# Kernel tuning notes

Hardware: AMD Instinct MI355X
Metric: run time of the kernel (lower is better)

Reference implementation:

```python
import jax, jax.numpy as jnp
import numpy as np

ALPHA = 0.2  # LeakyReLU negative slope


def setup_inputs() -> dict:
    key = jax.random.key(0)
    k1, k2, k3, k4 = jax.random.split(key, 4)
    B, N, Fin, Fout = 8, 2048, 256, 256
    h = jax.random.normal(k1, (B, N, Fin), dtype=jnp.float32)
    # random 0/1 adjacency with guaranteed self-loops so every row has a neighbor
    adj = jax.random.randint(k2, (N, N), 0, 2).astype(jnp.float32)
    adj = jnp.maximum(adj, jnp.eye(N, dtype=jnp.float32))
    # xavier_uniform with gain=1.414
    def xavier(k, shape, gain=1.414):
        fan_in, fan_out = shape[0], shape[1]
        a = gain * np.sqrt(6.0 / (fan_in + fan_out))
        return jax.random.uniform(k, shape, dtype=jnp.float32, minval=-a, maxval=a)
    W = xavier(k3, (Fin, Fout))
    a = xavier(k4, (2 * Fout, 1))
    return {"h": h, "adj_matrix": adj, "W": W, "a": a}


def reference(h, adj_matrix, W, a):
    # h: [B, N, Fin], adj_matrix: [N, N], W: [Fin, Fout], a: [2*Fout, 1]
    Fout = W.shape[1]
    Wh = jnp.einsum("bnf,fo->bno", h, W)            # [B, N, Fout]
    a1, a2 = a[:Fout, 0], a[Fout:, 0]                 # split additive attention vector
    # e[b,i,j] = leakyrelu(Wh[b,i]@a1 + Wh[b,j]@a2) — equals concat([Wh_i,Wh_j])@a
    s1 = Wh @ a1                                      # [B, N]
    s2 = Wh @ a2                                      # [B, N]
    e = s1[:, :, None] + s2[:, None, :]               # [B, N, N]
    e = jnp.where(e >= 0, e, ALPHA * e)               # LeakyReLU
    e = jnp.where(adj_matrix[None] == 0, -jnp.inf, e)  # mask non-edges
    attention = jax.nn.softmax(e, axis=-1)            # [B, N, N]
    # dropout is identity in eval mode (training=False)
    h_prime = jnp.einsum("bij,bjo->bio", attention, Wh)
    return h_prime
```

## Files before the change

### kernel.cpp

```cpp
#include <hip/hip_runtime.h>
#include <cstdint>

#define NN 2048
#define LOG2E 1.4426950408889634f

typedef __attribute__((ext_vector_type(8))) short bf16x8;
typedef __attribute__((ext_vector_type(4))) float f32x4;

__device__ __forceinline__ unsigned short f2bf(float x){
  union { float f; unsigned u; } v; v.f = x;
  unsigned r = v.u + 0x7FFFu + ((v.u >> 16) & 1u);
  return (unsigned short)(r >> 16);
}
__device__ __forceinline__ unsigned pack2(float a, float b){
  return (unsigned)f2bf(a) | ((unsigned)f2bf(b) << 16);
}
__device__ __forceinline__ unsigned permpack(unsigned hi, unsigned lo){
  return __builtin_amdgcn_perm(hi, lo, 0x07060302u);
}

__global__ __launch_bounds__(256) void k_prep(const float* __restrict__ adj,
                                              const float* __restrict__ W,
                                              unsigned long long* __restrict__ ab,
                                              unsigned short* __restrict__ Wt){
  int tid = threadIdx.x;
  if (blockIdx.x < 2048){
    int i = blockIdx.x;
    int w = tid >> 6, lane = tid & 63;
    #pragma unroll
    for (int seg = 0; seg < 8; seg++){
      int j = seg * 256 + tid;
      unsigned long long m = __ballot(adj[(size_t)i * NN + j] != 0.0f);
      if (lane == 0) ab[i * 32 + seg * 4 + w] = m;
    }
  } else {
    int g = (blockIdx.x - 2048) * 256 + tid;
    int o = g >> 8, k = g & 255;
    Wt[g] = f2bf(W[k * 256 + o]);
  }
}

__global__ __launch_bounds__(512, 2) void k_fused_gemm(const float* __restrict__ h,
                                                       const unsigned short* __restrict__ Wt,
                                                       const float* __restrict__ a,
                                                       unsigned short* __restrict__ WhT,
                                                       float* __restrict__ s1c,
                                                       float* __restrict__ s2c){
  __shared__ __align__(16) unsigned char As[2 * 8192];
  __shared__ __align__(16) unsigned short Ts[256 * 72];
  __shared__ float s1p[8][64], s2p[8][64];
  const int tid = threadIdx.x;
  const int r0 = blockIdx.x * 64;
  const int b  = r0 >> 11;
  const int i0 = r0 & (NN - 1);
  const int w = tid >> 6, lane = tid & 63, lhi = lane >> 4, llo = lane & 15;
  const int wc = w * 32;
  const int sit = w >> 1, skk = w & 1;
  const int srow = sit * 16 + llo;
  const int skol = skk * 32 + lhi * 8;

  f32x4 acc[4][2];
  #pragma unroll
  for (int i = 0; i < 4; i++)
    #pragma unroll
    for (int j = 0; j < 2; j++){ acc[i][j][0]=0.f; acc[i][j][1]=0.f; acc[i][j][2]=0.f; acc[i][j][3]=0.f; }

  float4 hv[4][2];
  #pragma unroll
  for (int t = 0; t < 4; t++){
    const float* hp = h + (size_t)(r0 + srow) * 256 + t * 64 + skol;
    hv[t][0] = *(const float4*)hp;
    hv[t][1] = *(const float4*)(hp + 4);
  }

  auto loadB = [&](int k0, bf16x8* dst){
    #pragma unroll
    for (int ot = 0; ot < 2; ot++)
      #pragma unroll
      for (int kk = 0; kk < 2; kk++)
        dst[ot * 2 + kk] = *(const bf16x8*)(Wt + (size_t)(wc + ot * 16 + llo) * 256 + k0 + kk * 32 + lhi * 8);
  };
  bf16x8 bfr[2][4];
  loadB(0, bfr[0]);

  #pragma unroll
  for (int t = 0; t < 4; t++){
    uint4 q = make_uint4(pack2(hv[t][0].x, hv[t][0].y), pack2(hv[t][0].z, hv[t][0].w),
                         pack2(hv[t][1].x, hv[t][1].y), pack2(hv[t][1].z, hv[t][1].w));
    *(uint4*)&As[(t & 1) * 8192 + w * 1024 + lane * 16] = q;
    __syncthreads();
    if (t < 3) loadB((t + 1) * 64, bfr[(t + 1) & 1]);
    bf16x8 af[2][4];
    #pragma unroll
    for (int kk = 0; kk < 2; kk++)
      #pragma unroll
      for (int it = 0; it < 4; it++)
        af[kk][it] = *(const bf16x8*)&As[(t & 1) * 8192 + (it * 2 + kk) * 1024 + lane * 16];
    #pragma unroll
    for (int kk = 0; kk < 2; kk++)
      #pragma unroll
      for (int it = 0; it < 4; it++)
        #pragma unroll
        for (int ot = 0; ot < 2; ot++)
          acc[it][ot] = __builtin_amdgcn_mfma_f32_16x16x32_bf16(af[kk][it], bfr[t & 1][ot * 2 + kk], acc[it][ot], 0, 0, 0);
  }

  float a1v[2], a2v[2];
  #pragma unroll
  for (int ot = 0; ot < 2; ot++){
    a1v[ot] = a[wc + ot * 16 + llo] * LOG2E;
    a2v[ot] = a[256 + wc + ot * 16 + llo] * LOG2E;
  }
  #pragma unroll
  for (int it = 0; it < 4; it++){
    #pragma unroll
    for (int q = 0; q < 4; q++){
      float p1 = acc[it][0][q] * a1v[0] + acc[it][1][q] * a1v[1];
      float p2 = acc[it][0][q] * a2v[0] + acc[it][1][q] * a2v[1];
      #pragma unroll
      for (int o = 1; o < 16; o <<= 1){ p1 += __shfl_xor(p1, o); p2 += __shfl_xor(p2, o); }
      if (llo == 0){
        s1p[w][it * 16 + lhi * 4 + q] = p1;
        s2p[w][it * 16 + lhi * 4 + q] = p2;
      }
    }
  }

  #pragma unroll
  for (int it = 0; it < 4; it++){
    #pragma unroll
    for (int ot = 0; ot < 2; ot++){
      int o = wc + ot * 16 + llo;
      uint2 u = make_uint2(pack2(acc[it][ot][0], acc[it][ot][1]),
                           pack2(acc[it][ot][2], acc[it][ot][3]));
      *(uint2*)&Ts[o * 72 + it * 16 + lhi * 4] = u;
    }
  }
  __syncthreads();

  if (tid < 64){
    float t1 = 0.f, t2 = 0.f;
    #pragma unroll
    for (int g = 0; g < 8; g++){ t1 += s1p[g][tid]; t2 += s2p[g][tid]; }
    s1c[r0 + tid] = t1;
    s2c[r0 + tid] = t2;
  }
  #pragma unroll
  for (int p = 0; p < 4; p++){
    int o = p * 64 + (tid >> 3), col = (tid & 7) * 8;
    *(uint4*)(WhT + (size_t)(b * 256 + o) * 2048 + i0 + col) = *(const uint4*)&Ts[o * 72 + col];
  }
}

__global__ __launch_bounds__(512, 2) void k_attn(const float* __restrict__ s1c,
                                                 const float* __restrict__ s2c,
                                                 const unsigned short* __restrict__ WhT,
                                                 const unsigned long long* __restrict__ ab,
                                                 float* __restrict__ out){
  __shared__ __align__(16) float s2s[2048];
  __shared__ __align__(16) unsigned char PsB[2 * 8192];
  __shared__ __align__(16) unsigned char bitsB[64 * 264];
  __shared__ float s1s[64], lin[64], red[8], rsp[8][64];
  const int tid = threadIdx.x;
  const int bid = blockIdx.x;
  const int b = bid & 7, i0 = (bid >> 3) * 64;
  const int w = tid >> 6, lane = tid & 63, lhi = lane >> 4, llo = lane & 15;
  const int wc = w * 32;
  const int sit = w >> 1, skk = w & 1;
  const int prow = sit * 16 + llo;

  float4 v = ((const float4*)(s2c + (size_t)b * NN))[tid];
  ((float4*)s2s)[tid] = v;
  float vmax = fmaxf(fmaxf(v.x, v.y), fmaxf(v.z, v.w));
  #pragma unroll
  for (int o = 32; o; o >>= 1) vmax = fmaxf(vmax, __shfl_xor(vmax, o));
  if (lane == 0) red[w] = vmax;
  if (tid < 64) s1s[tid] = s1c[(size_t)b * NN + i0 + tid];
  #pragma unroll
  for (int k = 0; k < 4; k++){
    int g = k * 512 + tid;
    unsigned long long mw = ab[(size_t)i0 * 32 + g];
    *(unsigned long long*)&bitsB[(g >> 5) * 264 + (g & 31) * 8] = mw;
  }
  __syncthreads();
  float m2 = red[0];
  #pragma unroll
  for (int g = 1; g < 8; g++) m2 = fmaxf(m2, red[g]);

  const float s1v = s1s[prow];
  const float xm = s1v + m2;
  const float mv = fmaxf(xm, 0.2f * xm);
  const float c1 = s1v - mv;
  const float c2 = 0.2f * s1v - mv;
  float rs = 0.f;

  f32x4 acc[4][2];
  #pragma unroll
  for (int i = 0; i < 4; i++)
    #pragma unroll
    for (int j = 0; j < 2; j++){ acc[i][j][0]=0.f; acc[i][j][1]=0.f; acc[i][j][2]=0.f; acc[i][j][3]=0.f; }

  auto loadB = [&](int j0, bf16x8* dst){
    #pragma unroll
    for (int ot = 0; ot < 2; ot++)
      #pragma unroll
      for (int kk = 0; kk < 2; kk++)
        dst[ot * 2 + kk] = *(const bf16x8*)(WhT + (size_t)(b * 256 + wc + ot * 16 + llo) * 2048 + j0 + kk * 32 + lhi * 8);
  };

  unsigned puq[4];
  auto computeP = [&](int tn){
    unsigned bits = bitsB[prow * 264 + tn * 8 + skk * 4 + lhi];
    const float* sp = &s2s[tn * 64 + skk * 32 + lhi * 8];
    float4 xa = *(const float4*)sp;
    float4 xb = *(const float4*)(sp + 4);
    float xs[8] = {xa.x, xa.y, xa.z, xa.w, xb.x, xb.y, xb.z, xb.w};
    unsigned pu[8];
    #pragma unroll
    for (int e = 0; e < 8; e++){
      float s2v = xs[e];
      float y = fmaxf(s2v + c1, __builtin_fmaf(0.2f, s2v, c2));
      float p = __builtin_amdgcn_exp2f(y);
      unsigned m = ((bits >> e) & 1u) ? 0xFFFF0000u : 0u;
      unsigned u = __float_as_uint(p) & m;
      rs += __uint_as_float(u);
      pu[e] = u;
    }
    puq[0] = permpack(pu[1], pu[0]); puq[1] = permpack(pu[3], pu[2]);
    puq[2] = permpack(pu[5], pu[4]); puq[3] = permpack(pu[7], pu[6]);
  };

  auto stageBody = [&](int t, int BUF, bf16x8* curB, bf16x8* nxtB, bool last){
    *(uint4*)&PsB[BUF * 8192 + w * 1024 + lane * 16] = *(uint4*)&puq[0];
    __syncthreads();
    if (!last) loadB((t + 1) * 64, nxtB);
    bf16x8 af[2][4];
    #pragma unroll
    for (int kk = 0; kk < 2; kk++)
      #pragma unroll
      for (int it = 0; it < 4; it++)
        af[kk][it] = *(const bf16x8*)&PsB[BUF * 8192 + (it * 2 + kk) * 1024 + lane * 16];
    if (!last) computeP(t + 1);
    #pragma unroll
    for (int kk = 0; kk < 2; kk++)
      #pragma unroll
      for (int it = 0; it < 4; it++)
        #pragma unroll
        for (int ot = 0; ot < 2; ot++)
          acc[it][ot] = __builtin_amdgcn_mfma_f32_16x16x32_bf16(af[kk][it], curB[ot * 2 + kk], acc[it][ot], 0, 0, 0);
  };

  bf16x8 bA[4], bB[4];
  loadB(0, bA);
  computeP(0);
  for (int t2 = 0; t2 < 32; t2 += 2){
    stageBody(t2,     0, bA, bB, false);
    stageBody(t2 + 1, 1, bB, bA, t2 + 1 == 31);
  }

  rs += __shfl_xor(rs, 16);
  rs += __shfl_xor(rs, 32);
  if (lhi == 0) rsp[w][prow] = rs;
  __syncthreads();
  if (tid < 64){
    int it = tid >> 4;
    lin[tid] = 1.0f / (rsp[it * 2][tid] + rsp[it * 2 + 1][tid]);
  }
  __syncthreads();

  #pragma unroll
  for (int it = 0; it < 4; it++){
    #pragma unroll
    for (int ot = 0; ot < 2; ot++){
      int col = wc + ot * 16 + llo;
      #pragma unroll
      for (int q = 0; q < 4; q++){
        int row = it * 16 + lhi * 4 + q;
        out[(size_t)(b * NN + i0 + row) * 256 + col] = acc[it][ot][q] * lin[row];
      }
    }
  }
}

extern "C" void kernel_launch(void* const* d_in, const int* in_sizes, int n_in,
                              void* d_out, int out_size, void* d_ws, size_t ws_size,
                              hipStream_t stream) {
  const float* h   = (const float*)d_in[0];
  const float* adj = (const float*)d_in[1];
  const float* W   = (const float*)d_in[2];
  const float* a   = (const float*)d_in[3];
  float* out = (float*)d_out;

  char* ws = (char*)d_ws;
  unsigned short* WhT      = (unsigned short*)(ws);
  unsigned short* Wt       = (unsigned short*)(ws + 8388608);
  unsigned long long* ab   = (unsigned long long*)(ws + 8519680);
  float* s1c               = (float*)(ws + 9043968);
  float* s2c               = (float*)(ws + 9109504);

  hipLaunchKernelGGL(k_prep,       dim3(2304), dim3(256), 0, stream, adj, W, ab, Wt);
  hipLaunchKernelGGL(k_fused_gemm, dim3(256),  dim3(512), 0, stream, h, Wt, a, WhT, s1c, s2c);
  hipLaunchKernelGGL(k_attn,       dim3(256),  dim3(512), 0, stream, s1c, s2c, WhT, ab, out);
}
```

Measured before the change: 135.2 us.

## Halve row tile to 32 rows per block, doubling grid size

Both the projection GEMM and the attention kernel now process 32 query rows per block instead of 64, so 512 blocks are launched instead of 256. Each wave computes half the rows and the staging layout splits each fragment across two waves. Launch bounds rise to 4 blocks per CU. The aim is to fill the MI355X's 256 CUs with more than one block each and improve latency hiding. The cost is that each WhT tile is reloaded by twice as many blocks, and each block does less MFMA work per barrier.

```diff
diff --git a/kernel.cpp b/kernel.cpp
--- a/kernel.cpp
+++ b/kernel.cpp
@@ -40,38 +40,36 @@
   }
 }
 
-__global__ __launch_bounds__(512, 2) void k_fused_gemm(const float* __restrict__ h,
+__global__ __launch_bounds__(512, 4) void k_fused_gemm(const float* __restrict__ h,
                                                        const unsigned short* __restrict__ Wt,
                                                        const float* __restrict__ a,
                                                        unsigned short* __restrict__ WhT,
                                                        float* __restrict__ s1c,
                                                        float* __restrict__ s2c){
-  __shared__ __align__(16) unsigned char As[2 * 8192];
-  __shared__ __align__(16) unsigned short Ts[256 * 72];
-  __shared__ float s1p[8][64], s2p[8][64];
+  __shared__ __align__(16) unsigned char As[2 * 4096];
+  __shared__ __align__(16) unsigned short Ts[256 * 40];
+  __shared__ float s1p[8][32], s2p[8][32];
   const int tid = threadIdx.x;
-  const int r0 = blockIdx.x * 64;
+  const int r0 = blockIdx.x * 32;
   const int b  = r0 >> 11;
   const int i0 = r0 & (NN - 1);
   const int w = tid >> 6, lane = tid & 63, lhi = lane >> 4, llo = lane & 15;
   const int wc = w * 32;
-  const int sit = w >> 1, skk = w & 1;
+  const int sit = w >> 2, skk = (w >> 1) & 1, sh2 = w & 1;
+  const int sfrag = sit * 2 + skk;
   const int srow = sit * 16 + llo;
-  const int skol = skk * 32 + lhi * 8;
-
-  f32x4 acc[4][2];
-  #pragma unroll
-  for (int i = 0; i < 4; i++)
+  const int skol = skk * 32 + lhi * 8 + sh2 * 4;
+
+  f32x4 acc[2][2];
+  #pragma unroll
+  for (int i = 0; i < 2; i++)
     #pragma unroll
     for (int j = 0; j < 2; j++){ acc[i][j][0]=0.f; acc[i][j][1]=0.f; acc[i][j][2]=0.f; acc[i][j][3]=0.f; }
 
-  float4 hv[4][2];
-  #pragma unroll
-  for (int t = 0; t < 4; t++){
-    const float* hp = h + (size_t)(r0 + srow) * 256 + t * 64 + skol;
-    hv[t][0] = *(const float4*)hp;
-    hv[t][1] = *(const float4*)(hp + 4);
-  }
+  float4 hv[4];
+  #pragma unroll
+  for (int t = 0; t < 4; t++)
+    hv[t] = *(const float4*)(h + (size_t)(r0 + srow) * 256 + t * 64 + skol);
 
   auto loadB = [&](int k0, bf16x8* dst){
     #pragma unroll
@@ -85,21 +83,20 @@
 
   #pragma unroll
   for (int t = 0; t < 4; t++){
-    uint4 q = make_uint4(pack2(hv[t][0].x, hv[t][0].y), pack2(hv[t][0].z, hv[t][0].w),
-                         pack2(hv[t][1].x, hv[t][1].y), pack2(hv[t][1].z, hv[t][1].w));
-    *(uint4*)&As[(t & 1) * 8192 + w * 1024 + lane * 16] = q;
+    *(uint2*)&As[(t & 1) * 4096 + sfrag * 1024 + lane * 16 + sh2 * 8] =
+        make_uint2(pack2(hv[t].x, hv[t].y), pack2(hv[t].z, hv[t].w));
     __syncthreads();
     if (t < 3) loadB((t + 1) * 64, bfr[(t + 1) & 1]);
-    bf16x8 af[2][4];
+    bf16x8 af[2][2];
     #pragma unroll
     for (int kk = 0; kk < 2; kk++)
       #pragma unroll
-      for (int it = 0; it < 4; it++)
-        af[kk][it] = *(const bf16x8*)&As[(t & 1) * 8192 + (it * 2 + kk) * 1024 + lane * 16];
+      for (int it = 0; it < 2; it++)
+        af[kk][it] = *(const bf16x8*)&As[(t & 1) * 4096 + (it * 2 + kk) * 1024 + lane * 16];
     #pragma unroll
     for (int kk = 0; kk < 2; kk++)
       #pragma unroll
-      for (int it = 0; it < 4; it++)
+      for (int it = 0; it < 2; it++)
         #pragma unroll
         for (int ot = 0; ot < 2; ot++)
           acc[it][ot] = __builtin_amdgcn_mfma_f32_16x16x32_bf16(af[kk][it], bfr[t & 1][ot * 2 + kk], acc[it][ot], 0, 0, 0);
@@ -112,7 +109,7 @@
     a2v[ot] = a[256 + wc + ot * 16 + llo] * LOG2E;
   }
   #pragma unroll
-  for (int it = 0; it < 4; it++){
+  for (int it = 0; it < 2; it++){
     #pragma unroll
     for (int q = 0; q < 4; q++){
       float p1 = acc[it][0][q] * a1v[0] + acc[it][1][q] * a1v[1];
@@ -127,18 +124,18 @@
   }
 
   #pragma unroll
-  for (int it = 0; it < 4; it++){
+  for (int it = 0; it < 2; it++){
     #pragma unroll
     for (int ot = 0; ot < 2; ot++){
       int o = wc + ot * 16 + llo;
-      uint2 u = make_uint2(pack2(acc[it][ot][0], acc[it][ot][1]),
-                           pack2(acc[it][ot][2], acc[it][ot][3]));
-      *(uint2*)&Ts[o * 72 + it * 16 + lhi * 4] = u;
+      *(uint2*)&Ts[o * 40 + it * 16 + lhi * 4] =
+          make_uint2(pack2(acc[it][ot][0], acc[it][ot][1]),
+                     pack2(acc[it][ot][2], acc[it][ot][3]));
     }
   }
   __syncthreads();
 
-  if (tid < 64){
+  if (tid < 32){
     float t1 = 0.f, t2 = 0.f;
     #pragma unroll
     for (int g = 0; g < 8; g++){ t1 += s1p[g][tid]; t2 += s2p[g][tid]; }
@@ -146,27 +143,29 @@
     s2c[r0 + tid] = t2;
   }
   #pragma unroll
-  for (int p = 0; p < 4; p++){
-    int o = p * 64 + (tid >> 3), col = (tid & 7) * 8;
-    *(uint4*)(WhT + (size_t)(b * 256 + o) * 2048 + i0 + col) = *(const uint4*)&Ts[o * 72 + col];
-  }
-}
-
-__global__ __launch_bounds__(512, 2) void k_attn(const float* __restrict__ s1c,
+  for (int p = 0; p < 2; p++){
+    int idx = p * 512 + tid;
+    int o = idx >> 2, col = (idx & 3) * 8;
+    *(uint4*)(WhT + (size_t)(b * 256 + o) * 2048 + i0 + col) = *(const uint4*)&Ts[o * 40 + col];
+  }
+}
+
+__global__ __launch_bounds__(512, 4) void k_attn(const float* __restrict__ s1c,
                                                  const float* __restrict__ s2c,
                                                  const unsigned short* __restrict__ WhT,
                                                  const unsigned long long* __restrict__ ab,
                                                  float* __restrict__ out){
   __shared__ __align__(16) float s2s[2048];
-  __shared__ __align__(16) unsigned char PsB[2 * 8192];
-  __shared__ __align__(16) unsigned char bitsB[64 * 264];
-  __shared__ float s1s[64], lin[64], red[8], rsp[8][64];
+  __shared__ __align__(16) unsigned char PsB[2 * 4096];
+  __shared__ __align__(16) unsigned char bitsB[32 * 264];
+  __shared__ float s1s[32], lin[32], red[8], rsp[8][32];
   const int tid = threadIdx.x;
   const int bid = blockIdx.x;
-  const int b = bid & 7, i0 = (bid >> 3) * 64;
+  const int b = bid & 7, i0 = (bid >> 3) * 32;
   const int w = tid >> 6, lane = tid & 63, lhi = lane >> 4, llo = lane & 15;
   const int wc = w * 32;
-  const int sit = w >> 1, skk = w & 1;
+  const int sit = w >> 2, skk = (w >> 1) & 1, sh2 = w & 1;
+  const int sfrag = sit * 2 + skk;
   const int prow = sit * 16 + llo;
 
   float4 v = ((const float4*)(s2c + (size_t)b * NN))[tid];
@@ -175,9 +174,9 @@
   #pragma unroll
   for (int o = 32; o; o >>= 1) vmax = fmaxf(vmax, __shfl_xor(vmax, o));
   if (lane == 0) red[w] = vmax;
-  if (tid < 64) s1s[tid] = s1c[(size_t)b * NN + i0 + tid];
-  #pragma unroll
-  for (int k = 0; k < 4; k++){
+  if (tid < 32) s1s[tid] = s1c[(size_t)b * NN + i0 + tid];
+  #pragma unroll
+  for (int k = 0; k < 2; k++){
     int g = k * 512 + tid;
     unsigned long long mw = ab[(size_t)i0 * 32 + g];
     *(unsigned long long*)&bitsB[(g >> 5) * 264 + (g & 31) * 8] = mw;
@@ -194,9 +193,9 @@
   const float c2 = 0.2f * s1v - mv;
   float rs = 0.f;
 
-  f32x4 acc[4][2];
-  #pragma unroll
-  for (int i = 0; i < 4; i++)
+  f32x4 acc[2][2];
+  #pragma unroll
+  for (int i = 0; i < 2; i++)
     #pragma unroll
     for (int j = 0; j < 2; j++){ acc[i][j][0]=0.f; acc[i][j][1]=0.f; acc[i][j][2]=0.f; acc[i][j][3]=0.f; }
 
@@ -208,16 +207,15 @@
         dst[ot * 2 + kk] = *(const bf16x8*)(WhT + (size_t)(b * 256 + wc + ot * 16 + llo) * 2048 + j0 + kk * 32 + lhi * 8);
   };
 
-  unsigned puq[4];
+  unsigned puq[2];
   auto computeP = [&](int tn){
-    unsigned bits = bitsB[prow * 264 + tn * 8 + skk * 4 + lhi];
-    const float* sp = &s2s[tn * 64 + skk * 32 + lhi * 8];
+    unsigned bits = (bitsB[prow * 264 + tn * 8 + skk * 4 + lhi] >> (sh2 * 4)) & 0xFu;
+    const float* sp = &s2s[tn * 64 + skk * 32 + lhi * 8 + sh2 * 4];
     float4 xa = *(const float4*)sp;
-    float4 xb = *(const float4*)(sp + 4);
-    float xs[8] = {xa.x, xa.y, xa.z, xa.w, xb.x, xb.y, xb.z, xb.w};
-    unsigned pu[8];
-    #pragma unroll
-    for (int e = 0; e < 8; e++){
+    float xs[4] = {xa.x, xa.y, xa.z, xa.w};
+    unsigned pu[4];
+    #pragma unroll
+    for (int e = 0; e < 4; e++){
       float s2v = xs[e];
       float y = fmaxf(s2v + c1, __builtin_fmaf(0.2f, s2v, c2));
       float p = __builtin_amdgcn_exp2f(y);
@@ -227,24 +225,23 @@
       pu[e] = u;
     }
     puq[0] = permpack(pu[1], pu[0]); puq[1] = permpack(pu[3], pu[2]);
-    puq[2] = permpack(pu[5], pu[4]); puq[3] = permpack(pu[7], pu[6]);
   };
 
   auto stageBody = [&](int t, int BUF, bf16x8* curB, bf16x8* nxtB, bool last){
-    *(uint4*)&PsB[BUF * 8192 + w * 1024 + lane * 16] = *(uint4*)&puq[0];
+    *(uint2*)&PsB[BUF * 4096 + sfrag * 1024 + lane * 16 + sh2 * 8] = make_uint2(puq[0], puq[1]);
     __syncthreads();
     if (!last) loadB((t + 1) * 64, nxtB);
-    bf16x8 af[2][4];
+    bf16x8 af[2][2];
     #pragma unroll
     for (int kk = 0; kk < 2; kk++)
       #pragma unroll
-      for (int it = 0; it < 4; it++)
-        af[kk][it] = *(const bf16x8*)&PsB[BUF * 8192 + (it * 2 + kk) * 1024 + lane * 16];
+      for (int it = 0; it < 2; it++)
+        af[kk][it] = *(const bf16x8*)&PsB[BUF * 4096 + (it * 2 + kk) * 1024 + lane * 16];
     if (!last) computeP(t + 1);
     #pragma unroll
     for (int kk = 0; kk < 2; kk++)
       #pragma unroll
-      for (int it = 0; it < 4; it++)
+      for (int it = 0; it < 2; it++)
         #pragma unroll
         for (int ot = 0; ot < 2; ot++)
           acc[it][ot] = __builtin_amdgcn_mfma_f32_16x16x32_bf16(af[kk][it], curB[ot * 2 + kk], acc[it][ot], 0, 0, 0);
@@ -262,14 +259,14 @@
   rs += __shfl_xor(rs, 32);
   if (lhi == 0) rsp[w][prow] = rs;
   __syncthreads();
-  if (tid < 64){
-    int it = tid >> 4;
-    lin[tid] = 1.0f / (rsp[it * 2][tid] + rsp[it * 2 + 1][tid]);
+  if (tid < 32){
+    int g0 = (tid >> 4) * 4;
+    lin[tid] = 1.0f / (rsp[g0][tid] + rsp[g0 + 1][tid] + rsp[g0 + 2][tid] + rsp[g0 + 3][tid]);
   }
   __syncthreads();
 
   #pragma unroll
-  for (int it = 0; it < 4; it++){
+  for (int it = 0; it < 2; it++){
     #pragma unroll
     for (int ot = 0; ot < 2; ot++){
       int col = wc + ot * 16 + llo;
@@ -299,6 +296,6 @@
   float* s2c               = (float*)(ws + 9109504);
 
   hipLaunchKernelGGL(k_prep,       dim3(2304), dim3(256), 0, stream, adj, W, ab, Wt);
-  hipLaunchKernelGGL(k_fused_gemm, dim3(256),  dim3(512), 0, stream, h, Wt, a, WhT, s1c, s2c);
-  hipLaunchKernelGGL(k_attn,       dim3(256),  dim3(512), 0, stream, s1c, s2c, WhT, ab, out);
-}
+  hipLaunchKernelGGL(k_fused_gemm, dim3(512),  dim3(512), 0, stream, h, Wt, a, WhT, s1c, s2c);
+  hipLaunchKernelGGL(k_attn,       dim3(512),  dim3(512), 0, stream, s1c, s2c, WhT, ab, out);
+}
```

Result: slower. 157.3 us (+16.3%).

## Vectorize adjacency bitpacking and double attention k-tile per barrier

Applied to the files above, without the earlier changes.

The prep kernel now reads the adjacency with float4 loads and builds the bitmask through shuffle-based nibble merging, with each block handling four rows. That cuts the block count from 2048 to 512 mask blocks. The attention kernel processes 128 columns per stage instead of 64, with two P sub-tiles per LDS buffer. This halves the number of __syncthreads and gives the WhT loads more time to land. The cost is doubled B-fragment registers and LDS for P, which may lower occupancy or cause spills under the 512x2 launch bound.

```diff
diff --git a/kernel.cpp b/kernel.cpp
--- a/kernel.cpp
+++ b/kernel.cpp
@@ -23,18 +23,29 @@
                                               const float* __restrict__ W,
                                               unsigned long long* __restrict__ ab,
                                               unsigned short* __restrict__ Wt){
-  int tid = threadIdx.x;
-  if (blockIdx.x < 2048){
-    int i = blockIdx.x;
-    int w = tid >> 6, lane = tid & 63;
-    #pragma unroll
-    for (int seg = 0; seg < 8; seg++){
-      int j = seg * 256 + tid;
-      unsigned long long m = __ballot(adj[(size_t)i * NN + j] != 0.0f);
-      if (lane == 0) ab[i * 32 + seg * 4 + w] = m;
+  const int tid = threadIdx.x;
+  const int bid = blockIdx.x;
+  if (bid < 512){
+    const int lane = tid & 63;
+    unsigned* ab32 = (unsigned*)ab;
+    #pragma unroll
+    for (int r = 0; r < 4; r++){
+      const int row = bid * 4 + r;
+      #pragma unroll
+      for (int part = 0; part < 2; part++){
+        float4 v = ((const float4*)(adj + (size_t)row * NN))[part * 256 + tid];
+        unsigned n = (v.x != 0.f ? 1u : 0u) | (v.y != 0.f ? 2u : 0u)
+                   | (v.z != 0.f ? 4u : 0u) | (v.w != 0.f ? 8u : 0u);
+        unsigned m;
+        m = __shfl_xor(n, 1); n = (lane & 1) ? (m | (n << 4))  : (n | (m << 4));
+        m = __shfl_xor(n, 2); n = (lane & 2) ? (m | (n << 8))  : (n | (m << 8));
+        m = __shfl_xor(n, 4); n = (lane & 4) ? (m | (n << 16)) : (n | (m << 16));
+        if ((lane & 7) == 0)
+          ab32[row * 64 + part * 32 + (tid >> 3)] = n;
+      }
     }
   } else {
-    int g = (blockIdx.x - 2048) * 256 + tid;
+    int g = (bid - 512) * 256 + tid;
     int o = g >> 8, k = g & 255;
     Wt[g] = f2bf(W[k * 256 + o]);
   }
@@ -158,7 +169,7 @@
                                                  const unsigned long long* __restrict__ ab,
                                                  float* __restrict__ out){
   __shared__ __align__(16) float s2s[2048];
-  __shared__ __align__(16) unsigned char PsB[2 * 8192];
+  __shared__ __align__(16) unsigned char PsB[2 * 16384];
   __shared__ __align__(16) unsigned char bitsB[64 * 264];
   __shared__ float s1s[64], lin[64], red[8], rsp[8][64];
   const int tid = threadIdx.x;
@@ -167,6 +178,7 @@
   const int w = tid >> 6, lane = tid & 63, lhi = lane >> 4, llo = lane & 15;
   const int wc = w * 32;
   const int sit = w >> 1, skk = w & 1;
+  const int sfrag = sit * 2 + skk;
   const int prow = sit * 16 + llo;
 
   float4 v = ((const float4*)(s2c + (size_t)b * NN))[tid];
@@ -202,14 +214,16 @@
 
   auto loadB = [&](int j0, bf16x8* dst){
     #pragma unroll
-    for (int ot = 0; ot < 2; ot++)
-      #pragma unroll
-      for (int kk = 0; kk < 2; kk++)
-        dst[ot * 2 + kk] = *(const bf16x8*)(WhT + (size_t)(b * 256 + wc + ot * 16 + llo) * 2048 + j0 + kk * 32 + lhi * 8);
+    for (int jh = 0; jh < 2; jh++)
+      #pragma unroll
+      for (int ot = 0; ot < 2; ot++)
+        #pragma unroll
+        for (int kk = 0; kk < 2; kk++)
+          dst[jh * 4 + ot * 2 + kk] = *(const bf16x8*)(WhT + (size_t)(b * 256 + wc + ot * 16 + llo) * 2048 + j0 + jh * 64 + kk * 32 + lhi * 8);
   };
 
-  unsigned puq[4];
-  auto computeP = [&](int tn){
+  unsigned puq[8];
+  auto computeP = [&](int tn, unsigned* pq){
     unsigned bits = bitsB[prow * 264 + tn * 8 + skk * 4 + lhi];
     const float* sp = &s2s[tn * 64 + skk * 32 + lhi * 8];
     float4 xa = *(const float4*)sp;
@@ -226,21 +240,22 @@
       rs += __uint_as_float(u);
       pu[e] = u;
     }
-    puq[0] = permpack(pu[1], pu[0]); puq[1] = permpack(pu[3], pu[2]);
-    puq[2] = permpack(pu[5], pu[4]); puq[3] = permpack(pu[7], pu[6]);
+    pq[0] = permpack(pu[1], pu[0]); pq[1] = permpack(pu[3], pu[2]);
+    pq[2] = permpack(pu[5], pu[4]); pq[3] = permpack(pu[7], pu[6]);
   };
 
   auto stageBody = [&](int t, int BUF, bf16x8* curB, bf16x8* nxtB, bool last){
-    *(uint4*)&PsB[BUF * 8192 + w * 1024 + lane * 16] = *(uint4*)&puq[0];
+    *(uint4*)&PsB[BUF * 16384 +        sfrag * 1024 + lane * 16] = *(uint4*)&puq[0];
+    *(uint4*)&PsB[BUF * 16384 + 8192 + sfrag * 1024 + lane * 16] = *(uint4*)&puq[4];
     __syncthreads();
-    if (!last) loadB((t + 1) * 64, nxtB);
+    if (!last) loadB((t + 1) * 128, nxtB);
     bf16x8 af[2][4];
     #pragma unroll
     for (int kk = 0; kk < 2; kk++)
       #pragma unroll
       for (int it = 0; it < 4; it++)
-        af[kk][it] = *(const bf16x8*)&PsB[BUF * 8192 + (it * 2 + kk) * 1024 + lane * 16];
-    if (!last) computeP(t + 1);
+        af[kk][it] = *(const bf16x8*)&PsB[BUF * 16384 + (it * 2 + kk) * 1024 + lane * 16];
+    if (!last) computeP(2 * (t + 1), &puq[0]);
     #pragma unroll
     for (int kk = 0; kk < 2; kk++)
       #pragma unroll
@@ -248,14 +263,28 @@
         #pragma unroll
         for (int ot = 0; ot < 2; ot++)
           acc[it][ot] = __builtin_amdgcn_mfma_f32_16x16x32_bf16(af[kk][it], curB[ot * 2 + kk], acc[it][ot], 0, 0, 0);
+    #pragma unroll
+    for (int kk = 0; kk < 2; kk++)
+      #pragma unroll
+      for (int it = 0; it < 4; it++)
+        af[kk][it] = *(const bf16x8*)&PsB[BUF * 16384 + 8192 + (it * 2 + kk) * 1024 + lane * 16];
+    if (!last) computeP(2 * (t + 1) + 1, &puq[4]);
+    #pragma unroll
+    for (int kk = 0; kk < 2; kk++)
+      #pragma unroll
+      for (int it = 0; it < 4; it++)
+        #pragma unroll
+        for (int ot = 0; ot < 2; ot++)
+          acc[it][ot] = __builtin_amdgcn_mfma_f32_16x16x32_bf16(af[kk][it], curB[4 + ot * 2 + kk], acc[it][ot], 0, 0, 0);
   };
 
-  bf16x8 bA[4], bB[4];
+  bf16x8 bA[8], bB[8];
   loadB(0, bA);
-  computeP(0);
-  for (int t2 = 0; t2 < 32; t2 += 2){
+  computeP(0, &puq[0]);
+  computeP(1, &puq[4]);
+  for (int t2 = 0; t2 < 16; t2 += 2){
     stageBody(t2,     0, bA, bB, false);
-    stageBody(t2 + 1, 1, bB, bA, t2 + 1 == 31);
+    stageBody(t2 + 1, 1, bB, bA, t2 + 1 == 15);
   }
 
   rs += __shfl_xor(rs, 16);
@@ -298,7 +327,7 @@
   float* s1c               = (float*)(ws + 9043968);
   float* s2c               = (float*)(ws + 9109504);
 
-  hipLaunchKernelGGL(k_prep,       dim3(2304), dim3(256), 0, stream, adj, W, ab, Wt);
-  hipLaunchKernelGGL(k_fused_gemm, dim3(256),  dim3(512), 0, stream, h, Wt, a, WhT, s1c, s2c);
-  hipLaunchKernelGGL(k_attn,       dim3(256),  dim3(512), 0, stream, s1c, s2c, WhT, ab, out);
-}
+  hipLaunchKernelGGL(k_prep,       dim3(768), dim3(256), 0, stream, adj, W, ab, Wt);
+  hipLaunchKernelGGL(k_fused_gemm, dim3(256), dim3(512), 0, stream, h, Wt, a, WhT, s1c, s2c);
+  hipLaunchKernelGGL(k_attn,       dim3(256), dim3(512), 0, stream, s1c, s2c, WhT, ab, out);
+}
```

Result: faster. 130.7 us (-3.3%).
